# Kernel optimization log

Hardware: AMD Instinct MI355X
Metric: run time of the kernel (lower is better)

Reference implementation:

```python
import jax, jax.numpy as jnp
import numpy as np

B, T, D_MODEL, D_HIDDEN = 4, 8192, 1024, 1024
EPS = 1e-5

def setup_inputs() -> dict:
    key = jax.random.key(0)
    ks = jax.random.split(key, 8)
    s_in = 1.0 / np.sqrt(D_MODEL)
    s_h = 1.0 / np.sqrt(D_HIDDEN)
    return {
        "x": jax.random.normal(ks[0], (B, T, D_MODEL), jnp.float32),
        "W_ih": jax.random.uniform(ks[1], (D_MODEL, D_HIDDEN), jnp.float32, -s_in, s_in),
        "b_ih": jnp.zeros((D_HIDDEN,), jnp.float32),
        "W_gate": jax.random.uniform(ks[2], (D_MODEL, D_HIDDEN), jnp.float32, -s_in, s_in),
        "b_gate": jnp.zeros((D_HIDDEN,), jnp.float32),
        "log_a": jnp.full((D_HIDDEN,), -0.1, jnp.float32),
        "ln_g": jnp.ones((D_HIDDEN,), jnp.float32),
        "ln_b": jnp.zeros((D_HIDDEN,), jnp.float32),
        "W_out": jax.random.uniform(ks[3], (D_HIDDEN, D_HIDDEN), jnp.float32, -s_h, s_h),
        "b_out": jnp.zeros((D_HIDDEN,), jnp.float32),
        "W_proj": jax.random.uniform(ks[4], (D_HIDDEN, D_MODEL), jnp.float32, -s_h, s_h),
        "b_proj": jnp.zeros((D_MODEL,), jnp.float32),
    }

def _scan(alpha, beta):
    # h_t = alpha_t * h_{t-1} + beta_t, h_0 = 0, over axis 1 (time)
    def combine(c1, c2):
        a1, b1 = c1
        a2, b2 = c2
        return a2 * a1, a2 * b1 + b2
    _, h = jax.lax.associative_scan(combine, (alpha, beta), axis=1)
    return h

def reference(x, W_ih, b_ih, W_gate, b_gate, log_a, ln_g, ln_b, W_out, b_out, W_proj, b_proj):
    ih = jnp.einsum("btd,dh->bth", x, W_ih) + b_ih
    gate = jax.nn.sigmoid(jnp.einsum("btd,dh->bth", x, W_gate) + b_gate)
    a = jnp.exp(log_a)  # [H]
    alpha = (1.0 - gate) * a  # [B,T,H]
    beta = gate * ih
    h = _scan(alpha, beta)
    # LayerNorm over last dim
    mu = jnp.mean(h, axis=-1, keepdims=True)
    var = jnp.var(h, axis=-1, keepdims=True)
    hn = (h - mu) * jax.lax.rsqrt(var + EPS) * ln_g + ln_b
    out = jnp.einsum("bth,ho->bto", hn, W_out) + b_out
    return jnp.einsum("bth,hd->btd", out, W_proj) + b_proj
```

## Files before the change

### kernel.cpp

```cpp
#include <hip/hip_runtime.h>

typedef short bhalf8 __attribute__((ext_vector_type(8)));
typedef float floatx4 __attribute__((ext_vector_type(4)));
typedef unsigned short ushortx8 __attribute__((ext_vector_type(8)));

__device__ __forceinline__ unsigned short f2bf(float f){
  union { float f; unsigned int u; } v; v.f = f;
  unsigned int u = v.u;
  u += 0x7fffu + ((u >> 16) & 1u);
  return (unsigned short)(u >> 16);
}
__device__ __forceinline__ float bf2f(unsigned short u){
  union { unsigned int u; float f; } v; v.u = ((unsigned)u) << 16; return v.f;
}
__device__ __forceinline__ unsigned pack2(float a, float b){
  return (unsigned)f2bf(a) | ((unsigned)f2bf(b) << 16);
}

__device__ __forceinline__ void async16(const unsigned short* g, unsigned short* l){
  __builtin_amdgcn_global_load_lds(
      (const __attribute__((address_space(1))) void*)g,
      (__attribute__((address_space(3))) void*)l,
      16, 0, 0);
}

template<int EPI>
__global__ __launch_bounds__(256) void gemm_k(
    const unsigned short* __restrict__ Ab, const unsigned short* __restrict__ BT,
    const float* __restrict__ bias, float* __restrict__ Cf,
    unsigned short* __restrict__ Cb, int K, int ldc)
{
  __shared__ __align__(16) unsigned short As[128*64];
  __shared__ __align__(16) unsigned short Bs[128*64];
  const int tid = threadIdx.x;
  const int n0 = blockIdx.x * 128;
  const int m0 = blockIdx.y * 128;
  const int wid = tid >> 6, lane = tid & 63;
  const int wr = (wid >> 1) * 64, wc = (wid & 1) * 64;
  const int r16 = lane & 15, quad = lane >> 4;
  const int ldsbase = (tid & ~63) * 8;

  const unsigned short* pA[4];
  const unsigned short* pB[4];
  #pragma unroll
  for (int i = 0; i < 4; ++i) {
    int p = tid + i*256;
    int row = p >> 3;
    int cp = (p & 7) ^ (row & 7);
    pA[i] = Ab + (size_t)(m0+row)*K + cp*8;
    pB[i] = BT + (size_t)(n0+row)*K + cp*8;
  }
  int aoff[2][4], boff[2][4];
  #pragma unroll
  for (int ks = 0; ks < 2; ++ks){
    #pragma unroll
    for (int mi = 0; mi < 4; ++mi){
      int row = wr + mi*16 + r16;
      aoff[ks][mi] = (row*8 + ((ks*4+quad) ^ (row&7))) * 8;
    }
    #pragma unroll
    for (int ni = 0; ni < 4; ++ni){
      int row = wc + ni*16 + r16;
      boff[ks][ni] = (row*8 + ((ks*4+quad) ^ (row&7))) * 8;
    }
  }

  floatx4 acc[4][4];
  #pragma unroll
  for (int i=0;i<4;i++)
    #pragma unroll
    for (int j2=0;j2<4;j2++) acc[i][j2] = {0.f,0.f,0.f,0.f};

  for (int k0 = 0; k0 < K; k0 += 64) {
    #pragma unroll
    for (int i = 0; i < 4; ++i) async16(pA[i], &As[ldsbase + i*2048]);
    #pragma unroll
    for (int i = 0; i < 4; ++i) async16(pB[i], &Bs[ldsbase + i*2048]);
    __syncthreads();
    #pragma unroll
    for (int ks = 0; ks < 2; ++ks) {
      bhalf8 aF[4], bF[4];
      #pragma unroll
      for (int mi=0;mi<4;++mi) aF[mi] = *(const bhalf8*)&As[aoff[ks][mi]];
      #pragma unroll
      for (int ni=0;ni<4;++ni) bF[ni] = *(const bhalf8*)&Bs[boff[ks][ni]];
      #pragma unroll
      for (int mi=0;mi<4;++mi)
        #pragma unroll
        for (int ni=0;ni<4;++ni)
          acc[mi][ni] = __builtin_amdgcn_mfma_f32_16x16x32_bf16(aF[mi], bF[ni], acc[mi][ni], 0, 0, 0);
    }
    __syncthreads();
    #pragma unroll
    for (int i = 0; i < 4; ++i) { pA[i] += 64; pB[i] += 64; }
  }

  #pragma unroll
  for (int mi=0;mi<4;++mi)
    #pragma unroll
    for (int ni=0;ni<4;++ni)
      #pragma unroll
      for (int rr=0;rr<4;++rr){
        int m = m0 + wr + mi*16 + quad*4 + rr;
        int n = n0 + wc + ni*16 + r16;
        float val = acc[mi][ni][rr];
        if (EPI == 0) Cf[(size_t)m*ldc + n] = val;
        else if (EPI == 1) Cf[(size_t)m*ldc + n] = val + bias[n];
        else if (EPI == 3) Cb[(size_t)m*ldc + n] = f2bf(val + bias[n]);
        else Cb[(size_t)n*ldc + m] = f2bf(val);
      }
}

__global__ __launch_bounds__(256) void prep_all(
    const float* __restrict__ W_ih, const float* __restrict__ W_gate,
    const float* __restrict__ W_proj, const float* __restrict__ W_out,
    const float* __restrict__ b_out, const float* __restrict__ b_proj,
    const float* __restrict__ log_a, const float* __restrict__ b_ih,
    const float* __restrict__ b_gate,
    unsigned short* __restrict__ WcatT, unsigned short* __restrict__ WprojT,
    unsigned short* __restrict__ Woutb,
    float* __restrict__ b_comb, float* __restrict__ a_vec, float* __restrict__ bcat)
{
  __shared__ float tile[32][33];
  const int blk = blockIdx.x;
  const int tid = threadIdx.x;
  if (blk < 3072) {
    const int which = blk >> 10;
    const int t = blk & 1023;
    const float* src = (which == 0) ? W_ih : (which == 1) ? W_gate : W_proj;
    unsigned short* dst = (which == 0) ? WcatT : (which == 1) ? (WcatT + 1024*1024) : WprojT;
    const int c0 = (t & 31) * 32, r0 = (t >> 5) * 32;
    const int tx = tid & 31, ty = tid >> 5;
    #pragma unroll
    for (int i = 0; i < 32; i += 8)
      tile[ty+i][tx] = src[(size_t)(r0+ty+i)*1024 + c0+tx];
    __syncthreads();
    #pragma unroll
    for (int i = 0; i < 32; i += 8)
      dst[(size_t)(c0+ty+i)*1024 + r0+tx] = f2bf(tile[tx][ty+i]);
  } else if (blk < 4096) {
    int idx = ((blk - 3072)*256 + tid) * 4;
    float4 v = *(const float4*)(W_out + idx);
    uint2 p;
    p.x = pack2(v.x, v.y);
    p.y = pack2(v.z, v.w);
    *(uint2*)(Woutb + idx) = p;
  } else {
    int d = (blk - 4096)*256 + tid;
    if (d < 1024) {
      float acc = b_proj[d];
      for (int e = 0; e < 1024; ++e)
        acc += b_out[e] * W_proj[(size_t)e*1024 + d];
      b_comb[d] = acc;
      a_vec[d] = __expf(log_a[d]);
      bcat[d] = b_ih[d];
    } else {
      bcat[d] = b_gate[d-1024];
    }
  }
}

__global__ __launch_bounds__(256) void cvt_f32_bf16(const float* __restrict__ src,
                                                    unsigned short* __restrict__ dst)
{
  int idx = (blockIdx.x*256 + threadIdx.x) * 4;
  float4 v = *(const float4*)(src + idx);
  uint2 p;
  p.x = pack2(v.x, v.y);
  p.y = pack2(v.z, v.w);
  *(uint2*)(dst + idx) = p;
}

#define CHUNK 32
#define NCHUNK 256

__device__ __forceinline__ void ab_step(unsigned short iu, unsigned short gu,
                                        float a, float& al, float& be)
{
  float zi = bf2f(iu), zg = bf2f(gu);
  float g = 1.f / (1.f + __expf(-zg));
  al = (1.f - g) * a;
  be = g * zi;
}

__global__ __launch_bounds__(256, 4) void scan_phase1(const unsigned short* __restrict__ pre,
    const float* __restrict__ a_vec, float* __restrict__ AsT, float* __restrict__ SsT)
{
  __shared__ float sA[4][1024];
  __shared__ float sS[4][1024];
  int wid = threadIdx.x >> 6, lane = threadIdx.x & 63;
  int u = blockIdx.x*4 + wid;
  int b = u >> 8, c = u & (NCHUNK-1);
  int ch0 = lane*16;
  float a[16], A[16], S[16];
  #pragma unroll
  for (int q=0;q<4;++q) *(float4*)&a[q*4] = *(const float4*)(a_vec + ch0 + q*4);
  #pragma unroll
  for (int j=0;j<16;++j){ A[j]=1.f; S[j]=0.f; }
  size_t base = ((size_t)(b*8192 + c*CHUNK))*2048 + ch0;
  for (int t=0;t<CHUNK;++t){
    ushortx8 i0 = *(const ushortx8*)(pre + base);
    ushortx8 i1 = *(const ushortx8*)(pre + base + 8);
    ushortx8 g0 = *(const ushortx8*)(pre + base + 1024);
    ushortx8 g1 = *(const ushortx8*)(pre + base + 1032);
    #pragma unroll
    for (int j=0;j<8;++j){
      float al, be;
      ab_step(i0[j], g0[j], a[j], al, be);
      A[j] *= al; S[j] = al*S[j] + be;
      ab_step(i1[j], g1[j], a[j+8], al, be);
      A[j+8] *= al; S[j+8] = al*S[j+8] + be;
    }
    base += 2048;
  }
  #pragma unroll
  for (int j=0;j<16;++j){ sA[wid][ch0+j] = A[j]; sS[wid][ch0+j] = S[j]; }
  __syncthreads();
  const int bb = blockIdx.x >> 6;
  const int c0 = (blockIdx.x*4) & (NCHUNK-1);
  const int t = threadIdx.x;
  #pragma unroll
  for (int q=0;q<4;++q){
    int ch = t + q*256;
    float4 va = make_float4(sA[0][ch], sA[1][ch], sA[2][ch], sA[3][ch]);
    float4 vs = make_float4(sS[0][ch], sS[1][ch], sS[2][ch], sS[3][ch]);
    size_t o = ((size_t)(bb*1024 + ch))*NCHUNK + c0;
    *(float4*)(AsT + o) = va;
    *(float4*)(SsT + o) = vs;
  }
}

__global__ __launch_bounds__(256) void scan_phase2(const float* __restrict__ AsT,
    const float* __restrict__ SsT, float* __restrict__ carryT)
{
  int wid = threadIdx.x >> 6, lane = threadIdx.x & 63;
  int p = blockIdx.x*4 + wid;
  size_t base = (size_t)p*NCHUNK + lane*4;
  float4 a4 = *(const float4*)(AsT + base);
  float4 s4 = *(const float4*)(SsT + base);
  float A = a4.x, S = s4.x;
  A = a4.y*A; S = a4.y*S + s4.y;
  A = a4.z*A; S = a4.z*S + s4.z;
  A = a4.w*A; S = a4.w*S + s4.w;
  float iA = A, iS = S;
  #pragma unroll
  for (int d = 1; d < 64; d <<= 1) {
    float pA = __shfl_up(iA, d);
    float pS = __shfl_up(iS, d);
    if (lane >= d) { iS = iA*pS + iS; iA = iA*pA; }
  }
  float bA = __shfl_up(iA, 1);
  float bS = __shfl_up(iS, 1);
  if (lane == 0) { bA = 1.f; bS = 0.f; }
  float4 c4;
  c4.x = bS;
  bS = a4.x*bS + s4.x; bA = a4.x*bA;
  c4.y = bS;
  bS = a4.y*bS + s4.y; bA = a4.y*bA;
  c4.z = bS;
  bS = a4.z*bS + s4.z;
  c4.w = bS;
  *(float4*)(carryT + base) = c4;
}

__global__ __launch_bounds__(256, 4) void scan_phase3(const unsigned short* __restrict__ pre,
    const float* __restrict__ a_vec, const float* __restrict__ carryT,
    const float* __restrict__ ln_g, const float* __restrict__ ln_b,
    unsigned short* __restrict__ hn)
{
  int wid = threadIdx.x >> 6, lane = threadIdx.x & 63;
  int u = blockIdx.x*4 + wid;
  int b = u >> 8, c = u & (NCHUNK-1);
  int ch0 = lane*16;
  float a[16], h[16], g[16], lb[16];
  #pragma unroll
  for (int q=0;q<4;++q){
    *(float4*)&a[q*4]  = *(const float4*)(a_vec + ch0 + q*4);
    *(float4*)&g[q*4]  = *(const float4*)(ln_g + ch0 + q*4);
    *(float4*)&lb[q*4] = *(const float4*)(ln_b + ch0 + q*4);
  }
  #pragma unroll
  for (int j=0;j<16;++j)
    h[j] = carryT[((size_t)b*1024 + ch0 + j)*NCHUNK + c];
  size_t base  = ((size_t)(b*8192 + c*CHUNK))*2048 + ch0;
  size_t hbase = ((size_t)(b*8192 + c*CHUNK))*1024 + ch0;
  for (int t=0;t<CHUNK;++t){
    ushortx8 i0 = *(const ushortx8*)(pre + base);
    ushortx8 i1 = *(const ushortx8*)(pre + base + 8);
    ushortx8 g0 = *(const ushortx8*)(pre + base + 1024);
    ushortx8 g1 = *(const ushortx8*)(pre + base + 1032);
    float s = 0.f, s2 = 0.f;
    #pragma unroll
    for (int j=0;j<8;++j){
      float al, be;
      ab_step(i0[j], g0[j], a[j], al, be);
      h[j] = al*h[j] + be;
      s += h[j]; s2 += h[j]*h[j];
      ab_step(i1[j], g1[j], a[j+8], al, be);
      h[j+8] = al*h[j+8] + be;
      s += h[j+8]; s2 += h[j+8]*h[j+8];
    }
    #pragma unroll
    for (int off = 32; off > 0; off >>= 1) {
      s  += __shfl_xor(s,  off);
      s2 += __shfl_xor(s2, off);
    }
    float mu = s * (1.f/1024.f);
    float var = s2 * (1.f/1024.f) - mu*mu;
    float rstd = rsqrtf(var + 1e-5f);
    uint4 o0, o1;
    float v0, v1;
    v0 = (h[0]-mu)*rstd*g[0]+lb[0];  v1 = (h[1]-mu)*rstd*g[1]+lb[1];  o0.x = pack2(v0,v1);
    v0 = (h[2]-mu)*rstd*g[2]+lb[2];  v1 = (h[3]-mu)*rstd*g[3]+lb[3];  o0.y = pack2(v0,v1);
    v0 = (h[4]-mu)*rstd*g[4]+lb[4];  v1 = (h[5]-mu)*rstd*g[5]+lb[5];  o0.z = pack2(v0,v1);
    v0 = (h[6]-mu)*rstd*g[6]+lb[6];  v1 = (h[7]-mu)*rstd*g[7]+lb[7];  o0.w = pack2(v0,v1);
    v0 = (h[8]-mu)*rstd*g[8]+lb[8];  v1 = (h[9]-mu)*rstd*g[9]+lb[9];  o1.x = pack2(v0,v1);
    v0 = (h[10]-mu)*rstd*g[10]+lb[10]; v1 = (h[11]-mu)*rstd*g[11]+lb[11]; o1.y = pack2(v0,v1);
    v0 = (h[12]-mu)*rstd*g[12]+lb[12]; v1 = (h[13]-mu)*rstd*g[13]+lb[13]; o1.z = pack2(v0,v1);
    v0 = (h[14]-mu)*rstd*g[14]+lb[14]; v1 = (h[15]-mu)*rstd*g[15]+lb[15]; o1.w = pack2(v0,v1);
    *(uint4*)(hn + hbase)     = o0;
    *(uint4*)(hn + hbase + 8) = o1;
    base += 2048; hbase += 1024;
  }
}

extern "C" void kernel_launch(void* const* d_in, const int* in_sizes, int n_in,
                              void* d_out, int out_size, void* d_ws, size_t ws_size,
                              hipStream_t stream)
{
  const float* x      = (const float*)d_in[0];
  const float* W_ih   = (const float*)d_in[1];
  const float* b_ih   = (const float*)d_in[2];
  const float* W_gate = (const float*)d_in[3];
  const float* b_gate = (const float*)d_in[4];
  const float* log_a  = (const float*)d_in[5];
  const float* ln_g   = (const float*)d_in[6];
  const float* ln_b   = (const float*)d_in[7];
  const float* W_out  = (const float*)d_in[8];
  const float* b_out  = (const float*)d_in[9];
  const float* W_proj = (const float*)d_in[10];
  const float* b_proj = (const float*)d_in[11];
  float* out = (float*)d_out;

  char* ws = (char*)d_ws;
  size_t off = 0;
  auto alloc = [&](size_t bytes)->char* {
    char* p = ws + off; off += (bytes + 255) & ~(size_t)255; return p;
  };
  unsigned short* pre   = (unsigned short*)alloc((size_t)32768*2048*2);
  unsigned short* hn    = (unsigned short*)alloc((size_t)32768*1024*2);
  unsigned short* xb    = hn;
  unsigned short* WcatT = (unsigned short*)alloc((size_t)2048*1024*2);
  unsigned short* WprojT= (unsigned short*)alloc((size_t)1024*1024*2);
  unsigned short* Woutb = (unsigned short*)alloc((size_t)1024*1024*2);
  unsigned short* WcombT= (unsigned short*)alloc((size_t)1024*1024*2);
  float* AsT            = (float*)alloc((size_t)1024*1024*4);
  float* SsT            = (float*)alloc((size_t)1024*1024*4);
  float* carryT         = (float*)alloc((size_t)1024*1024*4);
  float* b_comb         = (float*)alloc(1024*4);
  float* a_vec          = (float*)alloc(1024*4);
  float* bcat           = (float*)alloc(2048*4);

  prep_all<<<4104, 256, 0, stream>>>(W_ih, W_gate, W_proj, W_out, b_out, b_proj,
                                     log_a, b_ih, b_gate,
                                     WcatT, WprojT, Woutb, b_comb, a_vec, bcat);
  cvt_f32_bf16<<<32768, 256, 0, stream>>>(x, xb);
  gemm_k<2><<<dim3(8,8), 256, 0, stream>>>(Woutb, WprojT, nullptr, nullptr, WcombT, 1024, 1024);
  gemm_k<3><<<dim3(16,256), 256, 0, stream>>>(xb, WcatT, bcat, nullptr, pre, 1024, 2048);
  scan_phase1<<<256, 256, 0, stream>>>(pre, a_vec, AsT, SsT);
  scan_phase2<<<1024, 256, 0, stream>>>(AsT, SsT, carryT);
  scan_phase3<<<256, 256, 0, stream>>>(pre, a_vec, carryT, ln_g, ln_b, hn);
  gemm_k<1><<<dim3(8,256), 256, 0, stream>>>(hn, WcombT, b_comb, out, nullptr, 1024, 1024);
}
```

Measured before the change: 658.3 us.

## Halve scan chunk size, parallelize bias fold, merge x conversion into prep

The chunked scan now uses 16-step chunks (512 per batch), which doubles the blocks in scan phases 1 and 3 to raise occupancy on a 256-CU GPU. Phase 2 scans 8 chunk summaries per lane to match. The serial 1024-long b_out·W_proj reduction is split into 16 partial segments in prep_all and summed in phase 2. The x-to-bf16 conversion is merged into prep_all to save one launch. In exchange, the carry arrays are twice as large and phase 2 does more work per lane.

Result: faster. 618.5 us (-6.0%).

```diff
diff --git a/kernel.cpp b/kernel.cpp
--- a/kernel.cpp
+++ b/kernel.cpp
@@ -114,12 +114,12 @@
 __global__ __launch_bounds__(256) void prep_all(
     const float* __restrict__ W_ih, const float* __restrict__ W_gate,
     const float* __restrict__ W_proj, const float* __restrict__ W_out,
-    const float* __restrict__ b_out, const float* __restrict__ b_proj,
+    const float* __restrict__ b_out,
     const float* __restrict__ log_a, const float* __restrict__ b_ih,
-    const float* __restrict__ b_gate,
+    const float* __restrict__ b_gate, const float* __restrict__ x,
     unsigned short* __restrict__ WcatT, unsigned short* __restrict__ WprojT,
-    unsigned short* __restrict__ Woutb,
-    float* __restrict__ b_comb, float* __restrict__ a_vec, float* __restrict__ bcat)
+    unsigned short* __restrict__ Woutb, unsigned short* __restrict__ xb,
+    float* __restrict__ Pc, float* __restrict__ a_vec, float* __restrict__ bcat)
 {
   __shared__ float tile[32][33];
   const int blk = blockIdx.x;
@@ -145,34 +145,36 @@
     p.x = pack2(v.x, v.y);
     p.y = pack2(v.z, v.w);
     *(uint2*)(Woutb + idx) = p;
-  } else {
-    int d = (blk - 4096)*256 + tid;
+  } else if (blk < 4160) {
+    int blk2 = blk - 4096;
+    int dgrp = blk2 >> 4, seg = blk2 & 15;
+    int d = dgrp*256 + tid;
+    int e0 = seg*64;
+    float acc = 0.f;
+    #pragma unroll 8
+    for (int e = 0; e < 64; ++e)
+      acc += b_out[e0+e] * W_proj[(size_t)(e0+e)*1024 + d];
+    Pc[seg*1024 + d] = acc;
+  } else if (blk < 4168) {
+    int d = (blk - 4160)*256 + tid;
     if (d < 1024) {
-      float acc = b_proj[d];
-      for (int e = 0; e < 1024; ++e)
-        acc += b_out[e] * W_proj[(size_t)e*1024 + d];
-      b_comb[d] = acc;
       a_vec[d] = __expf(log_a[d]);
       bcat[d] = b_ih[d];
     } else {
       bcat[d] = b_gate[d-1024];
     }
-  }
-}
-
-__global__ __launch_bounds__(256) void cvt_f32_bf16(const float* __restrict__ src,
-                                                    unsigned short* __restrict__ dst)
-{
-  int idx = (blockIdx.x*256 + threadIdx.x) * 4;
-  float4 v = *(const float4*)(src + idx);
-  uint2 p;
-  p.x = pack2(v.x, v.y);
-  p.y = pack2(v.z, v.w);
-  *(uint2*)(dst + idx) = p;
-}
-
-#define CHUNK 32
-#define NCHUNK 256
+  } else {
+    int idx = ((blk - 4168)*256 + tid) * 4;
+    float4 v = *(const float4*)(x + idx);
+    uint2 p;
+    p.x = pack2(v.x, v.y);
+    p.y = pack2(v.z, v.w);
+    *(uint2*)(xb + idx) = p;
+  }
+}
+
+#define CHUNK 16
+#define NCHUNK 512
 
 __device__ __forceinline__ void ab_step(unsigned short iu, unsigned short gu,
                                         float a, float& al, float& be)
@@ -190,7 +192,7 @@
   __shared__ float sS[4][1024];
   int wid = threadIdx.x >> 6, lane = threadIdx.x & 63;
   int u = blockIdx.x*4 + wid;
-  int b = u >> 8, c = u & (NCHUNK-1);
+  int b = u >> 9, c = u & (NCHUNK-1);
   int ch0 = lane*16;
   float a[16], A[16], S[16];
   #pragma unroll
@@ -216,7 +218,7 @@
   #pragma unroll
   for (int j=0;j<16;++j){ sA[wid][ch0+j] = A[j]; sS[wid][ch0+j] = S[j]; }
   __syncthreads();
-  const int bb = blockIdx.x >> 6;
+  const int bb = blockIdx.x >> 7;
   const int c0 = (blockIdx.x*4) & (NCHUNK-1);
   const int t = threadIdx.x;
   #pragma unroll
@@ -231,17 +233,25 @@
 }
 
 __global__ __launch_bounds__(256) void scan_phase2(const float* __restrict__ AsT,
-    const float* __restrict__ SsT, float* __restrict__ carryT)
+    const float* __restrict__ SsT, float* __restrict__ carryT,
+    const float* __restrict__ Pc, const float* __restrict__ b_proj,
+    float* __restrict__ b_comb)
 {
   int wid = threadIdx.x >> 6, lane = threadIdx.x & 63;
   int p = blockIdx.x*4 + wid;
-  size_t base = (size_t)p*NCHUNK + lane*4;
-  float4 a4 = *(const float4*)(AsT + base);
-  float4 s4 = *(const float4*)(SsT + base);
-  float A = a4.x, S = s4.x;
-  A = a4.y*A; S = a4.y*S + s4.y;
-  A = a4.z*A; S = a4.z*S + s4.z;
-  A = a4.w*A; S = a4.w*S + s4.w;
+  size_t base = (size_t)p*NCHUNK + lane*8;
+  float4 a0 = *(const float4*)(AsT + base);
+  float4 a1 = *(const float4*)(AsT + base + 4);
+  float4 s0 = *(const float4*)(SsT + base);
+  float4 s1 = *(const float4*)(SsT + base + 4);
+  float A = a0.x, S = s0.x;
+  A = a0.y*A; S = a0.y*S + s0.y;
+  A = a0.z*A; S = a0.z*S + s0.z;
+  A = a0.w*A; S = a0.w*S + s0.w;
+  A = a1.x*A; S = a1.x*S + s1.x;
+  A = a1.y*A; S = a1.y*S + s1.y;
+  A = a1.z*A; S = a1.z*S + s1.z;
+  A = a1.w*A; S = a1.w*S + s1.w;
   float iA = A, iS = S;
   #pragma unroll
   for (int d = 1; d < 64; d <<= 1) {
@@ -249,18 +259,30 @@
     float pS = __shfl_up(iS, d);
     if (lane >= d) { iS = iA*pS + iS; iA = iA*pA; }
   }
-  float bA = __shfl_up(iA, 1);
   float bS = __shfl_up(iS, 1);
-  if (lane == 0) { bA = 1.f; bS = 0.f; }
-  float4 c4;
-  c4.x = bS;
-  bS = a4.x*bS + s4.x; bA = a4.x*bA;
-  c4.y = bS;
-  bS = a4.y*bS + s4.y; bA = a4.y*bA;
-  c4.z = bS;
-  bS = a4.z*bS + s4.z;
-  c4.w = bS;
-  *(float4*)(carryT + base) = c4;
+  if (lane == 0) bS = 0.f;
+  float4 c0v, c1v;
+  c0v.x = bS; bS = a0.x*bS + s0.x;
+  c0v.y = bS; bS = a0.y*bS + s0.y;
+  c0v.z = bS; bS = a0.z*bS + s0.z;
+  c0v.w = bS; bS = a0.w*bS + s0.w;
+  c1v.x = bS; bS = a1.x*bS + s1.x;
+  c1v.y = bS; bS = a1.y*bS + s1.y;
+  c1v.z = bS; bS = a1.z*bS + s1.z;
+  c1v.w = bS;
+  *(float4*)(carryT + base)     = c0v;
+  *(float4*)(carryT + base + 4) = c1v;
+
+  if (blockIdx.x == 0) {
+    #pragma unroll
+    for (int q = 0; q < 4; ++q) {
+      int d = threadIdx.x + q*256;
+      float acc = b_proj[d];
+      #pragma unroll
+      for (int s = 0; s < 16; ++s) acc += Pc[s*1024 + d];
+      b_comb[d] = acc;
+    }
+  }
 }
 
 __global__ __launch_bounds__(256, 4) void scan_phase3(const unsigned short* __restrict__ pre,
@@ -270,7 +292,7 @@
 {
   int wid = threadIdx.x >> 6, lane = threadIdx.x & 63;
   int u = blockIdx.x*4 + wid;
-  int b = u >> 8, c = u & (NCHUNK-1);
+  int b = u >> 9, c = u & (NCHUNK-1);
   int ch0 = lane*16;
   float a[16], h[16], g[16], lb[16];
   #pragma unroll
@@ -354,21 +376,22 @@
   unsigned short* WprojT= (unsigned short*)alloc((size_t)1024*1024*2);
   unsigned short* Woutb = (unsigned short*)alloc((size_t)1024*1024*2);
   unsigned short* WcombT= (unsigned short*)alloc((size_t)1024*1024*2);
-  float* AsT            = (float*)alloc((size_t)1024*1024*4);
-  float* SsT            = (float*)alloc((size_t)1024*1024*4);
-  float* carryT         = (float*)alloc((size_t)1024*1024*4);
+  float* AsT            = (float*)alloc((size_t)4*1024*NCHUNK*4);
+  float* SsT            = (float*)alloc((size_t)4*1024*NCHUNK*4);
+  float* carryT         = (float*)alloc((size_t)4*1024*NCHUNK*4);
+  float* Pc             = (float*)alloc((size_t)16*1024*4);
   float* b_comb         = (float*)alloc(1024*4);
   float* a_vec          = (float*)alloc(1024*4);
   float* bcat           = (float*)alloc(2048*4);
 
-  prep_all<<<4104, 256, 0, stream>>>(W_ih, W_gate, W_proj, W_out, b_out, b_proj,
-                                     log_a, b_ih, b_gate,
-                                     WcatT, WprojT, Woutb, b_comb, a_vec, bcat);
-  cvt_f32_bf16<<<32768, 256, 0, stream>>>(x, xb);
+  prep_all<<<4168 + 32768, 256, 0, stream>>>(W_ih, W_gate, W_proj, W_out, b_out,
+                                             log_a, b_ih, b_gate, x,
+                                             WcatT, WprojT, Woutb, xb,
+                                             Pc, a_vec, bcat);
   gemm_k<2><<<dim3(8,8), 256, 0, stream>>>(Woutb, WprojT, nullptr, nullptr, WcombT, 1024, 1024);
   gemm_k<3><<<dim3(16,256), 256, 0, stream>>>(xb, WcatT, bcat, nullptr, pre, 1024, 2048);
-  scan_phase1<<<256, 256, 0, stream>>>(pre, a_vec, AsT, SsT);
-  scan_phase2<<<1024, 256, 0, stream>>>(AsT, SsT, carryT);
-  scan_phase3<<<256, 256, 0, stream>>>(pre, a_vec, carryT, ln_g, ln_b, hn);
+  scan_phase1<<<512, 256, 0, stream>>>(pre, a_vec, AsT, SsT);
+  scan_phase2<<<1024, 256, 0, stream>>>(AsT, SsT, carryT, Pc, b_proj, b_comb);
+  scan_phase3<<<512, 256, 0, stream>>>(pre, a_vec, carryT, ln_g, ln_b, hn);
   gemm_k<1><<<dim3(8,256), 256, 0, stream>>>(hn, WcombT, b_comb, out, nullptr, 1024, 1024);
 }
```
